# Performance work log

Hardware: AMD Instinct MI355X
Metric: run time of the kernel (lower is better)

The kernel has to match this reference:

```python
import jax, jax.numpy as jnp
import numpy as np

BN_EPS = 1e-3  # O-CNN default bn_eps


def setup_inputs() -> dict:
    key = jax.random.key(0)
    k1, k2, k3 = jax.random.split(key, 3)
    N, Cin, Cout, K = 100000, 32, 32, 27  # nodes, channels, 3x3x3 taps
    data_in = jax.random.normal(k1, (1, Cin, N, 1), dtype=jnp.float32)
    neigh = jax.random.randint(k2, (N, K), 0, N, dtype=jnp.int32)
    weight = jax.random.normal(k3, (K, Cin, Cout), dtype=jnp.float32) * 0.05
    gamma = jnp.ones((Cout,), dtype=jnp.float32)
    beta = jnp.zeros((Cout,), dtype=jnp.float32)
    return {"data_in": data_in, "neigh": neigh, "weight": weight,
            "gamma": gamma, "beta": beta}


def reference(data_in, neigh, weight, gamma, beta):
    # data_in: [1, Cin, N, 1] -> x: [N, Cin]
    x = data_in[0, :, :, 0].T
    # Octree conv: gather 27 neighbor features per node, then small matmul.
    col = x[neigh]                                   # [N, 27, Cin] (irregular gather)
    y = jnp.einsum('nkc,kcd->nd', col, weight)       # [N, Cout]
    # BatchNorm2d in training mode: stats over the N (spatial) axis.
    mean = jnp.mean(y, axis=0)
    var = jnp.mean(jnp.square(y - mean), axis=0)     # biased variance, as BN uses
    yn = (y - mean) * jax.lax.rsqrt(var + BN_EPS) * gamma + beta
    # back to O-CNN layout [1, Cout, N, 1]
    return yn.T[None, :, :, None]
```

## Files before the change

### kernel.cpp

```cpp
#include <hip/hip_runtime.h>

#define KK 27

typedef short bf16x8 __attribute__((ext_vector_type(8)));
typedef float f32x4  __attribute__((ext_vector_type(4)));

__device__ inline unsigned short f2bf(float f) {
    unsigned u = __float_as_uint(f);
    unsigned r = u + 0x7fffu + ((u >> 16) & 1u);
    return (unsigned short)(r >> 16);
}

__global__ __launch_bounds__(256) void xprep_k(const float* __restrict__ in,
                                               unsigned short* __restrict__ xTb, int N) {
    __shared__ float tile[32][33];
    int n0 = blockIdx.x * 32;
    int tx = threadIdx.x & 31;
    int ty = threadIdx.x >> 5;
#pragma unroll
    for (int c = ty; c < 32; c += 8) {
        int n = n0 + tx;
        tile[c][tx] = (n < N) ? in[(long)c * N + n] : 0.f;
    }
    __syncthreads();
#pragma unroll
    for (int nn = ty; nn < 32; nn += 8) {
        int n = n0 + nn;
        if (n < N) xTb[(long)n * 32 + tx] = f2bf(tile[tx][nn]);
    }
}

__global__ __launch_bounds__(256) void wprep_k(const float* __restrict__ w,
                                               unsigned short* __restrict__ wTb) {
    int k = blockIdx.x;
    for (int i = threadIdx.x; i < 1024; i += 256) {
        int cin = i >> 5, cout = i & 31;
        wTb[k * 1024 + cout * 32 + cin] = f2bf(w[k * 1024 + cin * 32 + cout]);
    }
}

__global__ __launch_bounds__(64, 4) void conv_k(const unsigned short* __restrict__ xTb,
                                                const int* __restrict__ neigh,
                                                const unsigned short* __restrict__ wTb,
                                                float* __restrict__ y,
                                                float* __restrict__ partial,
                                                int N, int nrows) {
    __shared__ float ct[32][33];

    const int L    = threadIdx.x;
    const int r16  = L & 15;
    const int quad = L >> 4;
    const int base = blockIdx.x * 32;
    const int n0 = base + r16;
    const int n1 = base + 16 + r16;
    const bool v0 = (n0 < N), v1 = (n1 < N);
    const long nb0 = (long)(v0 ? n0 : 0) * KK;
    const long nb1 = (long)(v1 ? n1 : 0) * KK;

    const bf16x8 zz = {0, 0, 0, 0, 0, 0, 0, 0};

    f32x4 acc00 = {0.f, 0.f, 0.f, 0.f};
    f32x4 acc01 = acc00, acc10 = acc00, acc11 = acc00;

    int ia = neigh[nb0];
    int ib = neigh[nb1];
    int ja = neigh[nb0 + 1];
    int jb = neigh[nb1 + 1];

    bf16x8 a0 = *(const bf16x8*)(xTb + (long)ia * 32 + quad * 8);
    bf16x8 a1 = *(const bf16x8*)(xTb + (long)ib * 32 + quad * 8);
    bf16x8 b0 = *(const bf16x8*)(wTb + r16 * 32 + quad * 8);
    bf16x8 b1 = *(const bf16x8*)(wTb + (16 + r16) * 32 + quad * 8);
    a0 = v0 ? a0 : zz;
    a1 = v1 ? a1 : zz;

#pragma unroll 1
    for (int k = 0; k < KK; ++k) {
        bf16x8 na0 = zz, na1 = zz, pb0 = zz, pb1 = zz;
        if (k < KK - 1) {
            na0 = *(const bf16x8*)(xTb + (long)ja * 32 + quad * 8);
            na1 = *(const bf16x8*)(xTb + (long)jb * 32 + quad * 8);
            const unsigned short* wn = wTb + (k + 1) * 1024;
            pb0 = *(const bf16x8*)(wn + r16 * 32 + quad * 8);
            pb1 = *(const bf16x8*)(wn + (16 + r16) * 32 + quad * 8);
            int kk = (k + 2 < KK) ? (k + 2) : (KK - 1);
            ja = neigh[nb0 + kk];
            jb = neigh[nb1 + kk];
        }

        acc00 = __builtin_amdgcn_mfma_f32_16x16x32_bf16(a0, b0, acc00, 0, 0, 0);
        acc01 = __builtin_amdgcn_mfma_f32_16x16x32_bf16(a0, b1, acc01, 0, 0, 0);
        acc10 = __builtin_amdgcn_mfma_f32_16x16x32_bf16(a1, b0, acc10, 0, 0, 0);
        acc11 = __builtin_amdgcn_mfma_f32_16x16x32_bf16(a1, b1, acc11, 0, 0, 0);

        if (k < KK - 1) {
            a0 = v0 ? na0 : zz;
            a1 = v1 ? na1 : zz;
            b0 = pb0;
            b1 = pb1;
        }
    }

    float s0 = 0.f, q0 = 0.f, s1 = 0.f, q1 = 0.f;
#pragma unroll
    for (int r = 0; r < 4; ++r) {
        s0 += acc00[r] + acc10[r];
        q0 += acc00[r] * acc00[r] + acc10[r] * acc10[r];
        s1 += acc01[r] + acc11[r];
        q1 += acc01[r] * acc01[r] + acc11[r] * acc11[r];
    }
#pragma unroll
    for (int off = 16; off < 64; off <<= 1) {
        s0 += __shfl_xor(s0, off, 64);
        q0 += __shfl_xor(q0, off, 64);
        s1 += __shfl_xor(s1, off, 64);
        q1 += __shfl_xor(q1, off, 64);
    }
    if (L < 16) {
        const int b = blockIdx.x;
        partial[(long)L * nrows + b]        = s0;
        partial[(long)(L + 16) * nrows + b] = s1;
        partial[(long)(L + 32) * nrows + b] = q0;
        partial[(long)(L + 48) * nrows + b] = q1;
    }

#pragma unroll
    for (int r = 0; r < 4; ++r) {
        ct[quad * 4 + r][r16]           = acc00[r];
        ct[quad * 4 + r][16 + r16]      = acc01[r];
        ct[16 + quad * 4 + r][r16]      = acc10[r];
        ct[16 + quad * 4 + r][16 + r16] = acc11[r];
    }
    __syncthreads();
    const int node = L & 31;
    const int half = L >> 5;
    const int gn = base + node;
#pragma unroll
    for (int i = 0; i < 16; ++i) {
        const int cout = i * 2 + half;
        if (gn < N) y[(long)cout * N + gn] = ct[node][cout];
    }
}

__global__ __launch_bounds__(256) void stats1_k(const float* __restrict__ partial,
                                                int nrows, float* __restrict__ tot) {
    __shared__ float red[256];
    const int col = blockIdx.x;
    const float* row = partial + (long)col * nrows;
    float s = 0.f;
    for (int r = threadIdx.x; r < nrows; r += 256) s += row[r];
    red[threadIdx.x] = s;
    __syncthreads();
    for (int w = 128; w >= 64; w >>= 1) {
        if (threadIdx.x < w) red[threadIdx.x] += red[threadIdx.x + w];
        __syncthreads();
    }
    if (threadIdx.x < 64) {
        float v = red[threadIdx.x];
#pragma unroll
        for (int off = 1; off < 64; off <<= 1) v += __shfl_xor(v, off, 64);
        if (threadIdx.x == 0) tot[col] = v;
    }
}

__global__ __launch_bounds__(256) void norm_k(float* __restrict__ y,
                                              const float* __restrict__ tot,
                                              const float* __restrict__ gamma,
                                              const float* __restrict__ beta, int N) {
    const int d = blockIdx.y;
    const float mean = tot[d] / (float)N;
    const float var  = tot[d + 32] / (float)N - mean * mean;
    const float sc   = gamma[d] * rsqrtf(var + 1e-3f);
    const float sh   = beta[d] - mean * sc;

    int i = blockIdx.x * blockDim.x + threadIdx.x;
    int base = i * 4;
    if (base + 3 < N) {
        float4* p = (float4*)(y + (long)d * N + base);
        float4 v = *p;
        v.x = fmaf(v.x, sc, sh);
        v.y = fmaf(v.y, sc, sh);
        v.z = fmaf(v.z, sc, sh);
        v.w = fmaf(v.w, sc, sh);
        *p = v;
    } else if (base < N) {
        for (int t = base; t < N; ++t) y[(long)d * N + t] = fmaf(y[(long)d * N + t], sc, sh);
    }
}

extern "C" void kernel_launch(void* const* d_in, const int* in_sizes, int n_in,
                              void* d_out, int out_size, void* d_ws, size_t ws_size,
                              hipStream_t stream) {
    const float* data_in = (const float*)d_in[0];
    const int*   neigh   = (const int*)d_in[1];
    const float* weight  = (const float*)d_in[2];
    const float* gamma   = (const float*)d_in[3];
    const float* beta    = (const float*)d_in[4];
    float* out = (float*)d_out;

    const int N = in_sizes[1] / KK;
    const int nblk  = (N + 31) / 32;
    const int nrows = nblk;

    char* ws = (char*)d_ws;
    unsigned short* xTb = (unsigned short*)ws;
    unsigned short* wTb = (unsigned short*)(ws + (size_t)N * 64);
    float* partial = (float*)(ws + (size_t)N * 64 + 55296);
    float* tot     = partial + (size_t)64 * nrows;

    xprep_k<<<nblk, 256, 0, stream>>>(data_in, xTb, N);
    wprep_k<<<KK, 256, 0, stream>>>(weight, wTb);
    conv_k<<<nblk, 64, 0, stream>>>(xTb, neigh, wTb, out, partial, N, nrows);
    stats1_k<<<64, 256, 0, stream>>>(partial, nrows, tot);
    dim3 ngrid(((N + 3) / 4 + 255) / 256, 32);
    norm_k<<<ngrid, 256, 0, stream>>>(out, tot, gamma, beta, N);
}
```

Before: 136.9 us.

## Deepen gather prefetch pipeline, fuse prep kernels, atomic BN stats

Merges the x and weight prep kernels into one launch that also zeroes the stats buffer. The conv kernel now runs two waves per block and fully unrolls the tap loop, with a 4-deep ring of feature/weight loads and an 8-deep ring of neighbour-index loads. It replaces the per-block partial array plus separate reduction kernel with float atomicAdds into 64 totals. The aim is to hide gather latency and remove two launches, at the cost of more registers (the launch bound drops from 4 to 3 blocks) and heavy atomic contention on 64 addresses.

```diff
diff --git a/kernel.cpp b/kernel.cpp
--- a/kernel.cpp
+++ b/kernel.cpp
@@ -1,6 +1,8 @@
 #include <hip/hip_runtime.h>
 
 #define KK 27
+#define PD 4
+#define ID 8
 
 typedef short bf16x8 __attribute__((ext_vector_type(8)));
 typedef float f32x4  __attribute__((ext_vector_type(4)));
@@ -11,10 +13,22 @@
     return (unsigned short)(r >> 16);
 }
 
-__global__ __launch_bounds__(256) void xprep_k(const float* __restrict__ in,
-                                               unsigned short* __restrict__ xTb, int N) {
+__global__ __launch_bounds__(256) void prep_k(const float* __restrict__ in,
+                                              const float* __restrict__ w,
+                                              unsigned short* __restrict__ xTb,
+                                              unsigned short* __restrict__ wTb,
+                                              float* __restrict__ tot, int N) {
+    const int bx = blockIdx.x;
+    if (bx < KK) {
+        if (bx == 0 && threadIdx.x < 64) tot[threadIdx.x] = 0.f;
+        for (int i = threadIdx.x; i < 1024; i += 256) {
+            int cin = i >> 5, cout = i & 31;
+            wTb[bx * 1024 + cout * 32 + cin] = f2bf(w[bx * 1024 + cin * 32 + cout]);
+        }
+        return;
+    }
     __shared__ float tile[32][33];
-    int n0 = blockIdx.x * 32;
+    int n0 = (bx - KK) * 32;
     int tx = threadIdx.x & 31;
     int ty = threadIdx.x >> 5;
 #pragma unroll
@@ -30,75 +44,72 @@
     }
 }
 
-__global__ __launch_bounds__(256) void wprep_k(const float* __restrict__ w,
-                                               unsigned short* __restrict__ wTb) {
-    int k = blockIdx.x;
-    for (int i = threadIdx.x; i < 1024; i += 256) {
-        int cin = i >> 5, cout = i & 31;
-        wTb[k * 1024 + cout * 32 + cin] = f2bf(w[k * 1024 + cin * 32 + cout]);
-    }
-}
-
-__global__ __launch_bounds__(64, 4) void conv_k(const unsigned short* __restrict__ xTb,
-                                                const int* __restrict__ neigh,
-                                                const unsigned short* __restrict__ wTb,
-                                                float* __restrict__ y,
-                                                float* __restrict__ partial,
-                                                int N, int nrows) {
-    __shared__ float ct[32][33];
-
-    const int L    = threadIdx.x;
+__global__ __launch_bounds__(128, 3) void conv_k(const unsigned short* __restrict__ xTb,
+                                                 const int* __restrict__ neigh,
+                                                 const unsigned short* __restrict__ wTb,
+                                                 float* __restrict__ y,
+                                                 float* __restrict__ tot,
+                                                 int N) {
+    __shared__ float ct[2][32][33];
+
+    const int tid  = threadIdx.x;
+    const int L    = tid & 63;
+    const int wv   = tid >> 6;
     const int r16  = L & 15;
     const int quad = L >> 4;
-    const int base = blockIdx.x * 32;
-    const int n0 = base + r16;
-    const int n1 = base + 16 + r16;
-    const bool v0 = (n0 < N), v1 = (n1 < N);
-    const long nb0 = (long)(v0 ? n0 : 0) * KK;
-    const long nb1 = (long)(v1 ? n1 : 0) * KK;
-
-    const bf16x8 zz = {0, 0, 0, 0, 0, 0, 0, 0};
+    const int base = blockIdx.x * 64 + wv * 32;
+    const int n0c  = min(base + r16, N - 1);
+    const int n1c  = min(base + 16 + r16, N - 1);
+    const long nb0 = (long)n0c * KK;
+    const long nb1 = (long)n1c * KK;
 
     f32x4 acc00 = {0.f, 0.f, 0.f, 0.f};
     f32x4 acc01 = acc00, acc10 = acc00, acc11 = acc00;
 
-    int ia = neigh[nb0];
-    int ib = neigh[nb1];
-    int ja = neigh[nb0 + 1];
-    int jb = neigh[nb1 + 1];
-
-    bf16x8 a0 = *(const bf16x8*)(xTb + (long)ia * 32 + quad * 8);
-    bf16x8 a1 = *(const bf16x8*)(xTb + (long)ib * 32 + quad * 8);
-    bf16x8 b0 = *(const bf16x8*)(wTb + r16 * 32 + quad * 8);
-    bf16x8 b1 = *(const bf16x8*)(wTb + (16 + r16) * 32 + quad * 8);
-    a0 = v0 ? a0 : zz;
-    a1 = v1 ? a1 : zz;
-
-#pragma unroll 1
+    int    ja[ID], jb[ID];
+    bf16x8 A0[PD], A1[PD], B0[PD], B1[PD];
+
+#pragma unroll
+    for (int t = 0; t < ID; ++t) {
+        ja[t] = neigh[nb0 + t];
+        jb[t] = neigh[nb1 + t];
+    }
+#pragma unroll
+    for (int t = 0; t < PD; ++t) {
+        A0[t] = *(const bf16x8*)(xTb + (long)ja[t] * 32 + quad * 8);
+        A1[t] = *(const bf16x8*)(xTb + (long)jb[t] * 32 + quad * 8);
+        const unsigned short* wn = wTb + t * 1024;
+        B0[t] = *(const bf16x8*)(wn + r16 * 32 + quad * 8);
+        B1[t] = *(const bf16x8*)(wn + (16 + r16) * 32 + quad * 8);
+    }
+
+#pragma unroll
     for (int k = 0; k < KK; ++k) {
-        bf16x8 na0 = zz, na1 = zz, pb0 = zz, pb1 = zz;
-        if (k < KK - 1) {
-            na0 = *(const bf16x8*)(xTb + (long)ja * 32 + quad * 8);
-            na1 = *(const bf16x8*)(xTb + (long)jb * 32 + quad * 8);
-            const unsigned short* wn = wTb + (k + 1) * 1024;
-            pb0 = *(const bf16x8*)(wn + r16 * 32 + quad * 8);
-            pb1 = *(const bf16x8*)(wn + (16 + r16) * 32 + quad * 8);
-            int kk = (k + 2 < KK) ? (k + 2) : (KK - 1);
-            ja = neigh[nb0 + kk];
-            jb = neigh[nb1 + kk];
+        const int s = k % PD;
+        acc00 = __builtin_amdgcn_mfma_f32_16x16x32_bf16(A0[s], B0[s], acc00, 0, 0, 0);
+        acc01 = __builtin_amdgcn_mfma_f32_16x16x32_bf16(A0[s], B1[s], acc01, 0, 0, 0);
+        acc10 = __builtin_amdgcn_mfma_f32_16x16x32_bf16(A1[s], B0[s], acc10, 0, 0, 0);
+        acc11 = __builtin_amdgcn_mfma_f32_16x16x32_bf16(A1[s], B1[s], acc11, 0, 0, 0);
+
+        if (k + ID < KK) {
+            ja[k % ID] = neigh[nb0 + k + ID];
+            jb[k % ID] = neigh[nb1 + k + ID];
         }
-
-        acc00 = __builtin_amdgcn_mfma_f32_16x16x32_bf16(a0, b0, acc00, 0, 0, 0);
-        acc01 = __builtin_amdgcn_mfma_f32_16x16x32_bf16(a0, b1, acc01, 0, 0, 0);
-        acc10 = __builtin_amdgcn_mfma_f32_16x16x32_bf16(a1, b0, acc10, 0, 0, 0);
-        acc11 = __builtin_amdgcn_mfma_f32_16x16x32_bf16(a1, b1, acc11, 0, 0, 0);
-
-        if (k < KK - 1) {
-            a0 = v0 ? na0 : zz;
-            a1 = v1 ? na1 : zz;
-            b0 = pb0;
-            b1 = pb1;
+        if (k + PD < KK) {
+            const int ii = ja[(k + PD) % ID];
+            const int jj = jb[(k + PD) % ID];
+            A0[s] = *(const bf16x8*)(xTb + (long)ii * 32 + quad * 8);
+            A1[s] = *(const bf16x8*)(xTb + (long)jj * 32 + quad * 8);
+            const unsigned short* wn = wTb + (k + PD) * 1024;
+            B0[s] = *(const bf16x8*)(wn + r16 * 32 + quad * 8);
+            B1[s] = *(const bf16x8*)(wn + (16 + r16) * 32 + quad * 8);
         }
+    }
+
+#pragma unroll
+    for (int r = 0; r < 4; ++r) {
+        if (base + quad * 4 + r >= N)      { acc00[r] = 0.f; acc01[r] = 0.f; }
+        if (base + 16 + quad * 4 + r >= N) { acc10[r] = 0.f; acc11[r] = 0.f; }
     }
 
     float s0 = 0.f, q0 = 0.f, s1 = 0.f, q1 = 0.f;
@@ -117,19 +128,18 @@
         q1 += __shfl_xor(q1, off, 64);
     }
     if (L < 16) {
-        const int b = blockIdx.x;
-        partial[(long)L * nrows + b]        = s0;
-        partial[(long)(L + 16) * nrows + b] = s1;
-        partial[(long)(L + 32) * nrows + b] = q0;
-        partial[(long)(L + 48) * nrows + b] = q1;
+        atomicAdd(tot + L,      s0);
+        atomicAdd(tot + L + 16, s1);
+        atomicAdd(tot + L + 32, q0);
+        atomicAdd(tot + L + 48, q1);
     }
 
 #pragma unroll
     for (int r = 0; r < 4; ++r) {
-        ct[quad * 4 + r][r16]           = acc00[r];
-        ct[quad * 4 + r][16 + r16]      = acc01[r];
-        ct[16 + quad * 4 + r][r16]      = acc10[r];
-        ct[16 + quad * 4 + r][16 + r16] = acc11[r];
+        ct[wv][quad * 4 + r][r16]           = acc00[r];
+        ct[wv][quad * 4 + r][16 + r16]      = acc01[r];
+        ct[wv][16 + quad * 4 + r][r16]      = acc10[r];
+        ct[wv][16 + quad * 4 + r][16 + r16] = acc11[r];
     }
     __syncthreads();
     const int node = L & 31;
@@ -138,28 +148,7 @@
 #pragma unroll
     for (int i = 0; i < 16; ++i) {
         const int cout = i * 2 + half;
-        if (gn < N) y[(long)cout * N + gn] = ct[node][cout];
-    }
-}
-
-__global__ __launch_bounds__(256) void stats1_k(const float* __restrict__ partial,
-                                                int nrows, float* __restrict__ tot) {
-    __shared__ float red[256];
-    const int col = blockIdx.x;
-    const float* row = partial + (long)col * nrows;
-    float s = 0.f;
-    for (int r = threadIdx.x; r < nrows; r += 256) s += row[r];
-    red[threadIdx.x] = s;
-    __syncthreads();
-    for (int w = 128; w >= 64; w >>= 1) {
-        if (threadIdx.x < w) red[threadIdx.x] += red[threadIdx.x + w];
-        __syncthreads();
-    }
-    if (threadIdx.x < 64) {
-        float v = red[threadIdx.x];
-#pragma unroll
-        for (int off = 1; off < 64; off <<= 1) v += __shfl_xor(v, off, 64);
-        if (threadIdx.x == 0) tot[col] = v;
+        if (gn < N) y[(long)cout * N + gn] = ct[wv][node][cout];
     }
 }
 
@@ -199,19 +188,16 @@
     float* out = (float*)d_out;
 
     const int N = in_sizes[1] / KK;
-    const int nblk  = (N + 31) / 32;
-    const int nrows = nblk;
+    const int nblk32 = (N + 31) / 32;
+    const int nblk64 = (N + 63) / 64;
 
     char* ws = (char*)d_ws;
     unsigned short* xTb = (unsigned short*)ws;
     unsigned short* wTb = (unsigned short*)(ws + (size_t)N * 64);
-    float* partial = (float*)(ws + (size_t)N * 64 + 55296);
-    float* tot     = partial + (size_t)64 * nrows;
-
-    xprep_k<<<nblk, 256, 0, stream>>>(data_in, xTb, N);
-    wprep_k<<<KK, 256, 0, stream>>>(weight, wTb);
-    conv_k<<<nblk, 64, 0, stream>>>(xTb, neigh, wTb, out, partial, N, nrows);
-    stats1_k<<<64, 256, 0, stream>>>(partial, nrows, tot);
+    float* tot = (float*)(ws + (size_t)N * 64 + 55296);
+
+    prep_k<<<KK + nblk32, 256, 0, stream>>>(data_in, weight, xTb, wTb, tot, N);
+    conv_k<<<nblk64, 128, 0, stream>>>(xTb, neigh, wTb, out, tot, N);
     dim3 ngrid(((N + 3) / 4 + 255) / 256, 32);
     norm_k<<<ngrid, 256, 0, stream>>>(out, tot, gamma, beta, N);
 }
```

After: 192.0 us. 1.4x slower.
